# Kernel tuning notes

Hardware: AMD Instinct MI355X
Metric: run time of the kernel (lower is better)

## Reference

```python
import jax, jax.numpy as jnp
import numpy as np

B, S, D, H = 2, 2048, 768, 12
HD = D // H


def setup_inputs() -> dict:
    key = jax.random.key(0)
    ks = jax.random.split(key, 11)
    scale = 1.0 / np.sqrt(D)
    return {
        "query": jax.random.normal(ks[0], (B, S, D), jnp.float32),
        "key_": jax.random.normal(ks[1], (B, S, D), jnp.float32),
        "value": jax.random.normal(ks[2], (B, S, D), jnp.float32),
        "Wq": jax.random.normal(ks[3], (D, D), jnp.float32) * scale,
        "bq": jnp.zeros((D,), jnp.float32),
        "Wk": jax.random.normal(ks[4], (D, D), jnp.float32) * scale,
        "bk": jnp.zeros((D,), jnp.float32),
        "Wv": jax.random.normal(ks[5], (D, D), jnp.float32) * scale,
        "bv": jnp.zeros((D,), jnp.float32),
        "Wo": jax.random.normal(ks[6], (D, D), jnp.float32) * scale,
        "bo": jnp.zeros((D,), jnp.float32),
    }


def reference(query, key_, value, Wq, bq, Wk, bk, Wv, bv, Wo, bo):
    # Linear projections (W stored as [in, out]); dropout = identity (eval)
    def split_heads(x):
        # [B, S, D] -> [B, H, S, HD]
        return x.reshape(B, S, H, HD).transpose(0, 2, 1, 3)

    Q = split_heads(query @ Wq + bq)
    K = split_heads(key_ @ Wk + bk)
    V = split_heads(value @ Wv + bv)

    inv_sqrt_dk = 1.0 / jnp.sqrt(jnp.asarray(HD, Q.dtype))
    score = jnp.einsum("bhqd,bhkd->bhqk", Q, K) * inv_sqrt_dk  # [B,H,S,S]
    prob = jax.nn.softmax(score, axis=-1)  # source bug: mask is never applied
    out = jnp.einsum("bhqk,bhkd->bhqd", prob, V)  # [B,H,S,HD]
    out = out.transpose(0, 2, 1, 3).reshape(B, S, D)
    return out @ Wo + bo
```

## Files before the change

### kernel.cpp

```cpp
#include <hip/hip_runtime.h>
#include <hip/hip_bf16.h>

#define BB 2
#define SS 2048
#define DDIM 768
#define NH 12
#define HD 64
#define MTOT (BB*SS)

constexpr float QSCALE = 0.125f * 1.44269504088896340736f;

typedef __bf16 bf16_t;
typedef __bf16 bf16x8 __attribute__((ext_vector_type(8)));
typedef __bf16 bf16x4 __attribute__((ext_vector_type(4)));
typedef float  f32x4  __attribute__((ext_vector_type(4)));

static __device__ __forceinline__ f32x4 mfma16(bf16x8 a, bf16x8 b, f32x4 c) {
    return __builtin_amdgcn_mfma_f32_16x16x32_bf16(a, b, c, 0, 0, 0);
}

typedef __attribute__((address_space(3))) unsigned int lds_u32;
typedef __attribute__((address_space(1))) const unsigned int glob_u32;
static __device__ __forceinline__ void gload16(const bf16_t* g, bf16_t* l) {
    __builtin_amdgcn_global_load_lds((glob_u32*)g, (lds_u32*)l, 16, 0, 0);
}

__global__ __launch_bounds__(256) void prep_w(
    const float* __restrict__ Wq, const float* __restrict__ Wk,
    const float* __restrict__ Wv, const float* __restrict__ Wo,
    bf16_t* __restrict__ Wt)
{
    const int z = blockIdx.z, tid = threadIdx.x;
    __shared__ float tile[32][33];
    const float* W = (z == 0) ? Wq : (z == 1) ? Wk : (z == 2) ? Wv : Wo;
    int n0 = blockIdx.x * 32, k0 = blockIdx.y * 32;
    int tx = tid & 31, ty = tid >> 5;
#pragma unroll
    for (int i = 0; i < 4; i++) {
        int k = ty + i * 8;
        tile[k][tx] = W[(size_t)(k0 + k) * DDIM + n0 + tx];
    }
    __syncthreads();
    bf16_t* out = Wt + (size_t)z * DDIM * DDIM;
#pragma unroll
    for (int i = 0; i < 4; i++) {
        int n = ty + i * 8;
        out[(size_t)(n0 + n) * DDIM + k0 + tx] = (bf16_t)tile[tx][n];
    }
}

__global__ __launch_bounds__(256) void gemm_qkv(
    const float* __restrict__ qf32, const float* __restrict__ kf32,
    const float* __restrict__ vf,
    const float* __restrict__ bq, const float* __restrict__ bk, const float* __restrict__ bv,
    const bf16_t* __restrict__ Wt,
    bf16_t* __restrict__ Q, bf16_t* __restrict__ K, bf16_t* __restrict__ Vtg)
{
    __shared__ alignas(16) bf16_t As[128 * 64];
    __shared__ alignas(16) bf16_t Bs[128 * 64];
    const int z = blockIdx.z;
    const int m0 = blockIdx.y * 128, n0 = blockIdx.x * 128;
    const int tid = threadIdx.x, lane = tid & 63, w = tid >> 6;
    const int wm = (w >> 1) * 64, wn = (w & 1) * 64;
    const int quad = lane >> 4, l15 = lane & 15;

    const float* Af = (z == 0) ? qf32 : (z == 1) ? kf32 : vf;
    const bf16_t* Bt = Wt + (size_t)z * (DDIM * DDIM);
    const int arow = lane >> 3;
    const int asl  = ((lane & 7) ^ arow) * 8;
    bf16_t* BsW = &Bs[w * 2048];
    const int frow = tid >> 1, fhalf = tid & 1;

    f32x4 acc[4][4];
#pragma unroll
    for (int mt = 0; mt < 4; mt++)
#pragma unroll
        for (int nt = 0; nt < 4; nt++) { f32x4 zz = {0.f,0.f,0.f,0.f}; acc[mt][nt] = zz; }

    for (int k0 = 0; k0 < DDIM; k0 += 64) {
        __syncthreads();
        {
            const float* src = Af + (size_t)(m0 + frow) * DDIM + k0 + fhalf * 32;
            f32x4 v[8];
#pragma unroll
            for (int i = 0; i < 8; i++) v[i] = *(const f32x4*)(src + 4 * i);
            int rsw = frow & 7;
#pragma unroll
            for (int j = 0; j < 4; j++) {
                bf16x8 oj;
#pragma unroll
                for (int e = 0; e < 4; e++) {
                    oj[e]     = (bf16_t)v[2 * j][e];
                    oj[e + 4] = (bf16_t)v[2 * j + 1][e];
                }
                int phys = (fhalf * 4 + j) ^ rsw;
                *(bf16x8*)&As[frow * 64 + phys * 8] = oj;
            }
        }
        {
            const bf16_t* Bg = Bt + (size_t)(n0 + w * 32 + arow) * DDIM + k0 + asl;
#pragma unroll
            for (int i = 0; i < 4; i++)
                gload16(Bg + (size_t)(8 * i) * DDIM, BsW + 512 * i);
        }
        __syncthreads();

#pragma unroll
        for (int h = 0; h < 2; h++) {
            bf16x8 a[4], b[4];
#pragma unroll
            for (int mt = 0; mt < 4; mt++) {
                int r = wm + mt * 16 + l15;
                a[mt] = *(const bf16x8*)&As[r * 64 + (((h * 4 + quad) ^ (r & 7)) * 8)];
            }
#pragma unroll
            for (int nt = 0; nt < 4; nt++) {
                int r = wn + nt * 16 + l15;
                b[nt] = *(const bf16x8*)&Bs[r * 64 + (((h * 4 + quad) ^ (r & 7)) * 8)];
            }
#pragma unroll
            for (int mt = 0; mt < 4; mt++)
#pragma unroll
                for (int nt = 0; nt < 4; nt++)
                    acc[mt][nt] = mfma16(a[mt], b[nt], acc[mt][nt]);
        }
    }

    const float* bias = (z == 0) ? bq : (z == 1) ? bk : bv;
    float bvals[4];
#pragma unroll
    for (int nt = 0; nt < 4; nt++)
        bvals[nt] = bias[n0 + wn + nt * 16 + l15];

    if (z == 2) {
#pragma unroll
        for (int mt = 0; mt < 4; mt++) {
            int row0 = m0 + wm + mt * 16 + quad * 4;
#pragma unroll
            for (int nt = 0; nt < 4; nt++) {
                int col = n0 + wn + nt * 16 + l15;
                bf16x4 pk;
#pragma unroll
                for (int r = 0; r < 4; r++) pk[r] = (bf16_t)(acc[mt][nt][r] + bvals[nt]);
                *(bf16x4*)&Vtg[(size_t)col * MTOT + row0] = pk;
            }
        }
    } else {
        bf16_t* C = (z == 0) ? Q : K;
        float scale = (z == 0) ? QSCALE : 1.0f;
#pragma unroll
        for (int mt = 0; mt < 4; mt++) {
            int row0 = m0 + wm + mt * 16 + quad * 4;
#pragma unroll
            for (int nt = 0; nt < 4; nt++) {
                int col = n0 + wn + nt * 16 + l15;
#pragma unroll
                for (int r = 0; r < 4; r++)
                    C[(size_t)(row0 + r) * DDIM + col] = (bf16_t)((acc[mt][nt][r] + bvals[nt]) * scale);
            }
        }
    }
}

__global__ __launch_bounds__(256) void gemm_out(
    const bf16_t* __restrict__ Ab, const bf16_t* __restrict__ Bt,
    const float* __restrict__ bo, float* __restrict__ out)
{
    __shared__ alignas(16) bf16_t As[128 * 64];
    __shared__ alignas(16) bf16_t Bs[128 * 64];
    const int m0 = blockIdx.y * 128, n0 = blockIdx.x * 128;
    const int tid = threadIdx.x, lane = tid & 63, w = tid >> 6;
    const int wm = (w >> 1) * 64, wn = (w & 1) * 64;
    const int quad = lane >> 4, l15 = lane & 15;
    const int arow = lane >> 3;
    const int asl  = ((lane & 7) ^ arow) * 8;
    bf16_t* AsW = &As[w * 2048];
    bf16_t* BsW = &Bs[w * 2048];

    f32x4 acc[4][4];
#pragma unroll
    for (int mt = 0; mt < 4; mt++)
#pragma unroll
        for (int nt = 0; nt < 4; nt++) { f32x4 zz = {0.f,0.f,0.f,0.f}; acc[mt][nt] = zz; }

    for (int k0 = 0; k0 < DDIM; k0 += 64) {
        __syncthreads();
        {
            const bf16_t* Ag = Ab + (size_t)(m0 + w * 32 + arow) * DDIM + k0 + asl;
#pragma unroll
            for (int i = 0; i < 4; i++)
                gload16(Ag + (size_t)(8 * i) * DDIM, AsW + 512 * i);
            const bf16_t* Bg = Bt + (size_t)(n0 + w * 32 + arow) * DDIM + k0 + asl;
#pragma unroll
            for (int i = 0; i < 4; i++)
                gload16(Bg + (size_t)(8 * i) * DDIM, BsW + 512 * i);
        }
        __syncthreads();

#pragma unroll
        for (int h = 0; h < 2; h++) {
            bf16x8 a[4], b[4];
#pragma unroll
            for (int mt = 0; mt < 4; mt++) {
                int r = wm + mt * 16 + l15;
                a[mt] = *(const bf16x8*)&As[r * 64 + (((h * 4 + quad) ^ (r & 7)) * 8)];
            }
#pragma unroll
            for (int nt = 0; nt < 4; nt++) {
                int r = wn + nt * 16 + l15;
                b[nt] = *(const bf16x8*)&Bs[r * 64 + (((h * 4 + quad) ^ (r & 7)) * 8)];
            }
#pragma unroll
            for (int mt = 0; mt < 4; mt++)
#pragma unroll
                for (int nt = 0; nt < 4; nt++)
                    acc[mt][nt] = mfma16(a[mt], b[nt], acc[mt][nt]);
        }
    }

    float bvals[4];
#pragma unroll
    for (int nt = 0; nt < 4; nt++)
        bvals[nt] = bo[n0 + wn + nt * 16 + l15];
#pragma unroll
    for (int mt = 0; mt < 4; mt++) {
        int row0 = m0 + wm + mt * 16 + quad * 4;
#pragma unroll
        for (int nt = 0; nt < 4; nt++) {
            int col = n0 + wn + nt * 16 + l15;
#pragma unroll
            for (int r = 0; r < 4; r++)
                out[(size_t)(row0 + r) * DDIM + col] = acc[mt][nt][r] + bvals[nt];
        }
    }
}

__global__ __launch_bounds__(256) void attn_kernel(
    const bf16_t* __restrict__ Qb, const bf16_t* __restrict__ Kb,
    const bf16_t* __restrict__ Vtg, bf16_t* __restrict__ Ab)
{
    const int id = blockIdx.x;
    const int hb = id % 24, qi = id / 24;
    const int h = hb % NH, b = hb / NH;
    const int q0 = qi * 64;
    const int tid = threadIdx.x, lane = tid & 63, w = tid >> 6;
    const int quad = lane >> 4, l15 = lane & 15;

    __shared__ union {
        struct {
            alignas(16) bf16_t Ps[64][144];
        } a;
        struct {
            alignas(16) float Obuf[2][64][68];
            float Lb[4][64];
        } m;
    } u;

    bf16x8 qf[4][2];
#pragma unroll
    for (int qt = 0; qt < 4; qt++) {
        const bf16_t* src = Qb + (size_t)(b * SS + q0 + qt * 16 + l15) * DDIM + h * HD;
#pragma unroll
        for (int kh = 0; kh < 2; kh++)
            qf[qt][kh] = *(const bf16x8*)(src + kh * 32 + quad * 8);
    }

    f32x4 o[4][4];
#pragma unroll
    for (int dt = 0; dt < 4; dt++)
#pragma unroll
        for (int qt = 0; qt < 4; qt++) { f32x4 z = {0.f,0.f,0.f,0.f}; o[dt][qt] = z; }
    float l_s[4];
#pragma unroll
    for (int qt = 0; qt < 4; qt++) l_s[qt] = 0.f;

    const bf16_t* kfrag = Kb + (size_t)(b * SS + w * 32 + l15) * DDIM + h * HD + quad * 8;
    const bf16_t* vfrag = Vtg + (size_t)(h * HD + l15) * MTOT + b * SS + w * 32 + quad * 8;

    for (int kt0 = 0; kt0 < SS; kt0 += 128) {
        f32x4 s_[2][4];
#pragma unroll
        for (int kt = 0; kt < 2; kt++) {
            const bf16_t* kr = kfrag + (size_t)(kt0 + kt * 16) * DDIM;
            bf16x8 ak0 = *(const bf16x8*)(kr);
            bf16x8 ak1 = *(const bf16x8*)(kr + 32);
#pragma unroll
            for (int qt = 0; qt < 4; qt++) {
                f32x4 z = {0.f,0.f,0.f,0.f};
                z = mfma16(ak0, qf[qt][0], z);
                z = mfma16(ak1, qf[qt][1], z);
                s_[kt][qt] = z;
            }
        }

#pragma unroll
        for (int qt = 0; qt < 4; qt++) {
            float rs = l_s[qt];
#pragma unroll
            for (int kt = 0; kt < 2; kt++) {
                bf16x4 pk;
#pragma unroll
                for (int r = 0; r < 4; r++) {
                    float p = __builtin_amdgcn_exp2f(s_[kt][qt][r]);
                    rs += p;
                    pk[r] = (bf16_t)p;
                }
                *(bf16x4*)&u.a.Ps[qt * 16 + l15][w * 32 + kt * 16 + quad * 4] = pk;
            }
            l_s[qt] = rs;
        }

        bf16x8 av8[4], bp[4];
#pragma unroll
        for (int dt = 0; dt < 4; dt++)
            av8[dt] = *(const bf16x8*)(vfrag + (size_t)(dt * 16) * MTOT + kt0);
#pragma unroll
        for (int qt = 0; qt < 4; qt++)
            bp[qt] = *(const bf16x8*)&u.a.Ps[qt * 16 + l15][w * 32 + quad * 8];
#pragma unroll
        for (int dt = 0; dt < 4; dt++)
#pragma unroll
            for (int qt = 0; qt < 4; qt++)
                o[dt][qt] = mfma16(av8[dt], bp[qt], o[dt][qt]);
    }

#pragma unroll
    for (int qt = 0; qt < 4; qt++) {
        float rs = l_s[qt];
        rs += __shfl_xor(rs, 16, 64);
        rs += __shfl_xor(rs, 32, 64);
        l_s[qt] = rs;
    }
    __syncthreads();
    if (quad == 0) {
#pragma unroll
        for (int qt = 0; qt < 4; qt++)
            u.m.Lb[w][qt * 16 + l15] = l_s[qt];
    }
    __syncthreads();
    float lstar[4];
#pragma unroll
    for (int qt = 0; qt < 4; qt++) {
        int q = qt * 16 + l15;
        lstar[qt] = u.m.Lb[0][q] + u.m.Lb[1][q] + u.m.Lb[2][q] + u.m.Lb[3][q];
    }
    if (w >= 2) {
        float* dst = &u.m.Obuf[w - 2][lane][0];
#pragma unroll
        for (int dt = 0; dt < 4; dt++)
#pragma unroll
            for (int qt = 0; qt < 4; qt++)
                *(f32x4*)(dst + (dt * 4 + qt) * 4) = o[dt][qt];
    }
    __syncthreads();
    if (w < 2) {
        const float* src = &u.m.Obuf[w][lane][0];
#pragma unroll
        for (int dt = 0; dt < 4; dt++)
#pragma unroll
            for (int qt = 0; qt < 4; qt++)
                o[dt][qt] += *(const f32x4*)(src + (dt * 4 + qt) * 4);
    }
    __syncthreads();
    if (w == 1) {
        float* dst = &u.m.Obuf[0][lane][0];
#pragma unroll
        for (int dt = 0; dt < 4; dt++)
#pragma unroll
            for (int qt = 0; qt < 4; qt++)
                *(f32x4*)(dst + (dt * 4 + qt) * 4) = o[dt][qt];
    }
    __syncthreads();
    if (w == 0) {
        const float* src = &u.m.Obuf[0][lane][0];
#pragma unroll
        for (int dt = 0; dt < 4; dt++)
#pragma unroll
            for (int qt = 0; qt < 4; qt++)
                o[dt][qt] += *(const f32x4*)(src + (dt * 4 + qt) * 4);
#pragma unroll
        for (int qt = 0; qt < 4; qt++) {
            float inv = 1.f / lstar[qt];
            size_t rbase = (size_t)(b * SS + q0 + qt * 16 + l15) * DDIM + h * HD;
#pragma unroll
            for (int dt = 0; dt < 4; dt++) {
                bf16x4 pk;
#pragma unroll
                for (int r = 0; r < 4; r++) pk[r] = (bf16_t)(o[dt][qt][r] * inv);
                *(bf16x4*)&Ab[rbase + dt * 16 + quad * 4] = pk;
            }
        }
    }
}

extern "C" void kernel_launch(void* const* d_in, const int* in_sizes, int n_in,
                              void* d_out, int out_size, void* d_ws, size_t ws_size,
                              hipStream_t stream)
{
    const float* q  = (const float*)d_in[0];
    const float* k  = (const float*)d_in[1];
    const float* v  = (const float*)d_in[2];
    const float* Wq = (const float*)d_in[3];
    const float* bq = (const float*)d_in[4];
    const float* Wk = (const float*)d_in[5];
    const float* bk = (const float*)d_in[6];
    const float* Wv = (const float*)d_in[7];
    const float* bv = (const float*)d_in[8];
    const float* Wo = (const float*)d_in[9];
    const float* bo = (const float*)d_in[10];
    float* out = (float*)d_out;

    bf16_t* Wt  = (bf16_t*)d_ws;
    bf16_t* Ab  = Wt + (size_t)4 * DDIM * DDIM;
    bf16_t* Qs  = Ab + (size_t)MTOT * DDIM;
    bf16_t* Ks  = Qs + (size_t)MTOT * DDIM;
    bf16_t* Vtg = Ks + (size_t)MTOT * DDIM;

    prep_w<<<dim3(24, 24, 4), 256, 0, stream>>>(Wq, Wk, Wv, Wo, Wt);
    gemm_qkv<<<dim3(6, 32, 3), 256, 0, stream>>>(q, k, v, bq, bk, bv, Wt, Qs, Ks, Vtg);
    attn_kernel<<<dim3((SS / 64) * NH * BB), 256, 0, stream>>>(Qs, Ks, Vtg, Ab);
    gemm_out<<<dim3(6, 32), 256, 0, stream>>>(Ab, Wt + (size_t)3 * DDIM * DDIM, bo, out);
}
```

Baseline: 224.3 us.

## Shrink projection GEMM tiles, remap blocks across XCDs, prefetch fp32 A tiles

The QKV projection GEMM now uses 64x128 tiles, giving 1152 blocks instead of 576. The output GEMM uses 64x64 tiles, giving 768 blocks instead of 192. A block-index remap groups consecutive logical tiles onto the same XCD, which should improve L2 reuse. In the QKV kernel, the fp32 A loads for the next k-step are issued into registers before the MFMA loop so their latency overlaps compute. The aim is better CU occupancy and wave count on the MI355X, at the cost of less operand reuse per block and more redundant weight and activation loads.

Measured after the change: 197.9 us (median of 2 runs). -11.8%, faster.

```diff
diff --git a/kernel.cpp b/kernel.cpp
--- a/kernel.cpp
+++ b/kernel.cpp
@@ -56,12 +56,17 @@
     const bf16_t* __restrict__ Wt,
     bf16_t* __restrict__ Q, bf16_t* __restrict__ K, bf16_t* __restrict__ Vtg)
 {
-    __shared__ alignas(16) bf16_t As[128 * 64];
+    __shared__ alignas(16) bf16_t As[64 * 64];
     __shared__ alignas(16) bf16_t Bs[128 * 64];
-    const int z = blockIdx.z;
-    const int m0 = blockIdx.y * 128, n0 = blockIdx.x * 128;
+    const int gid = blockIdx.x;
+    const int lid = (gid & 7) * 144 + (gid >> 3);
+    const int z   = lid / 384;
+    const int rem = lid - z * 384;
+    const int mi  = rem / 6, ni = rem - mi * 6;
+    const int m0 = mi * 64, n0 = ni * 128;
+
     const int tid = threadIdx.x, lane = tid & 63, w = tid >> 6;
-    const int wm = (w >> 1) * 64, wn = (w & 1) * 64;
+    const int wm = (w >> 1) * 32, wn = (w & 1) * 64;
     const int quad = lane >> 4, l15 = lane & 15;
 
     const float* Af = (z == 0) ? qf32 : (z == 1) ? kf32 : vf;
@@ -69,33 +74,32 @@
     const int arow = lane >> 3;
     const int asl  = ((lane & 7) ^ arow) * 8;
     bf16_t* BsW = &Bs[w * 2048];
-    const int frow = tid >> 1, fhalf = tid & 1;
-
-    f32x4 acc[4][4];
-#pragma unroll
-    for (int mt = 0; mt < 4; mt++)
+    const int frow = tid >> 2, fq = tid & 3;
+    const int rsw = frow & 7;
+    const float* Abase = Af + (size_t)(m0 + frow) * DDIM + fq * 16;
+
+    f32x4 acc[2][4];
+#pragma unroll
+    for (int mt = 0; mt < 2; mt++)
 #pragma unroll
         for (int nt = 0; nt < 4; nt++) { f32x4 zz = {0.f,0.f,0.f,0.f}; acc[mt][nt] = zz; }
+
+    f32x4 vA[4];
+#pragma unroll
+    for (int i = 0; i < 4; i++) vA[i] = *(const f32x4*)(Abase + 4 * i);
 
     for (int k0 = 0; k0 < DDIM; k0 += 64) {
         __syncthreads();
-        {
-            const float* src = Af + (size_t)(m0 + frow) * DDIM + k0 + fhalf * 32;
-            f32x4 v[8];
-#pragma unroll
-            for (int i = 0; i < 8; i++) v[i] = *(const f32x4*)(src + 4 * i);
-            int rsw = frow & 7;
-#pragma unroll
-            for (int j = 0; j < 4; j++) {
-                bf16x8 oj;
-#pragma unroll
-                for (int e = 0; e < 4; e++) {
-                    oj[e]     = (bf16_t)v[2 * j][e];
-                    oj[e + 4] = (bf16_t)v[2 * j + 1][e];
-                }
-                int phys = (fhalf * 4 + j) ^ rsw;
-                *(bf16x8*)&As[frow * 64 + phys * 8] = oj;
-            }
+#pragma unroll
+        for (int j = 0; j < 2; j++) {
+            bf16x8 oj;
+#pragma unroll
+            for (int e = 0; e < 4; e++) {
+                oj[e]     = (bf16_t)vA[2 * j][e];
+                oj[e + 4] = (bf16_t)vA[2 * j + 1][e];
+            }
+            int phys = (fq * 2 + j) ^ rsw;
+            *(bf16x8*)&As[frow * 64 + phys * 8] = oj;
         }
         {
             const bf16_t* Bg = Bt + (size_t)(n0 + w * 32 + arow) * DDIM + k0 + asl;
@@ -104,12 +108,16 @@
                 gload16(Bg + (size_t)(8 * i) * DDIM, BsW + 512 * i);
         }
         __syncthreads();
-
+        if (k0 + 64 < DDIM) {
+            const float* nsrc = Abase + k0 + 64;
+#pragma unroll
+            for (int i = 0; i < 4; i++) vA[i] = *(const f32x4*)(nsrc + 4 * i);
+        }
 #pragma unroll
         for (int h = 0; h < 2; h++) {
-            bf16x8 a[4], b[4];
-#pragma unroll
-            for (int mt = 0; mt < 4; mt++) {
+            bf16x8 a[2], b[4];
+#pragma unroll
+            for (int mt = 0; mt < 2; mt++) {
                 int r = wm + mt * 16 + l15;
                 a[mt] = *(const bf16x8*)&As[r * 64 + (((h * 4 + quad) ^ (r & 7)) * 8)];
             }
@@ -119,7 +127,7 @@
                 b[nt] = *(const bf16x8*)&Bs[r * 64 + (((h * 4 + quad) ^ (r & 7)) * 8)];
             }
 #pragma unroll
-            for (int mt = 0; mt < 4; mt++)
+            for (int mt = 0; mt < 2; mt++)
 #pragma unroll
                 for (int nt = 0; nt < 4; nt++)
                     acc[mt][nt] = mfma16(a[mt], b[nt], acc[mt][nt]);
@@ -134,7 +142,7 @@
 
     if (z == 2) {
 #pragma unroll
-        for (int mt = 0; mt < 4; mt++) {
+        for (int mt = 0; mt < 2; mt++) {
             int row0 = m0 + wm + mt * 16 + quad * 4;
 #pragma unroll
             for (int nt = 0; nt < 4; nt++) {
@@ -149,7 +157,7 @@
         bf16_t* C = (z == 0) ? Q : K;
         float scale = (z == 0) ? QSCALE : 1.0f;
 #pragma unroll
-        for (int mt = 0; mt < 4; mt++) {
+        for (int mt = 0; mt < 2; mt++) {
             int row0 = m0 + wm + mt * 16 + quad * 4;
 #pragma unroll
             for (int nt = 0; nt < 4; nt++) {
@@ -166,67 +174,69 @@
     const bf16_t* __restrict__ Ab, const bf16_t* __restrict__ Bt,
     const float* __restrict__ bo, float* __restrict__ out)
 {
-    __shared__ alignas(16) bf16_t As[128 * 64];
-    __shared__ alignas(16) bf16_t Bs[128 * 64];
-    const int m0 = blockIdx.y * 128, n0 = blockIdx.x * 128;
+    __shared__ alignas(16) bf16_t As[64 * 64];
+    __shared__ alignas(16) bf16_t Bs[64 * 64];
+    const int gid = blockIdx.x;
+    const int lid = (gid & 7) * 96 + (gid >> 3);
+    const int mi  = lid / 12, ni = lid - mi * 12;
+    const int m0 = mi * 64, n0 = ni * 64;
+
     const int tid = threadIdx.x, lane = tid & 63, w = tid >> 6;
-    const int wm = (w >> 1) * 64, wn = (w & 1) * 64;
+    const int wm = (w >> 1) * 32, wn = (w & 1) * 32;
     const int quad = lane >> 4, l15 = lane & 15;
     const int arow = lane >> 3;
     const int asl  = ((lane & 7) ^ arow) * 8;
-    bf16_t* AsW = &As[w * 2048];
-    bf16_t* BsW = &Bs[w * 2048];
-
-    f32x4 acc[4][4];
-#pragma unroll
-    for (int mt = 0; mt < 4; mt++)
-#pragma unroll
-        for (int nt = 0; nt < 4; nt++) { f32x4 zz = {0.f,0.f,0.f,0.f}; acc[mt][nt] = zz; }
+    bf16_t* AsW = &As[w * 1024];
+    bf16_t* BsW = &Bs[w * 1024];
+
+    f32x4 acc[2][2];
+#pragma unroll
+    for (int mt = 0; mt < 2; mt++)
+#pragma unroll
+        for (int nt = 0; nt < 2; nt++) { f32x4 zz = {0.f,0.f,0.f,0.f}; acc[mt][nt] = zz; }
 
     for (int k0 = 0; k0 < DDIM; k0 += 64) {
         __syncthreads();
         {
-            const bf16_t* Ag = Ab + (size_t)(m0 + w * 32 + arow) * DDIM + k0 + asl;
-#pragma unroll
-            for (int i = 0; i < 4; i++)
-                gload16(Ag + (size_t)(8 * i) * DDIM, AsW + 512 * i);
-            const bf16_t* Bg = Bt + (size_t)(n0 + w * 32 + arow) * DDIM + k0 + asl;
-#pragma unroll
-            for (int i = 0; i < 4; i++)
-                gload16(Bg + (size_t)(8 * i) * DDIM, BsW + 512 * i);
+            const bf16_t* Ag = Ab + (size_t)(m0 + w * 16 + arow) * DDIM + k0 + asl;
+            gload16(Ag, AsW);
+            gload16(Ag + (size_t)8 * DDIM, AsW + 512);
+            const bf16_t* Bg = Bt + (size_t)(n0 + w * 16 + arow) * DDIM + k0 + asl;
+            gload16(Bg, BsW);
+            gload16(Bg + (size_t)8 * DDIM, BsW + 512);
         }
         __syncthreads();
 
 #pragma unroll
         for (int h = 0; h < 2; h++) {
-            bf16x8 a[4], b[4];
-#pragma unroll
-            for (int mt = 0; mt < 4; mt++) {
+            bf16x8 a[2], b[2];
+#pragma unroll
+            for (int mt = 0; mt < 2; mt++) {
                 int r = wm + mt * 16 + l15;
                 a[mt] = *(const bf16x8*)&As[r * 64 + (((h * 4 + quad) ^ (r & 7)) * 8)];
             }
 #pragma unroll
-            for (int nt = 0; nt < 4; nt++) {
+            for (int nt = 0; nt < 2; nt++) {
                 int r = wn + nt * 16 + l15;
                 b[nt] = *(const bf16x8*)&Bs[r * 64 + (((h * 4 + quad) ^ (r & 7)) * 8)];
             }
 #pragma unroll
-            for (int mt = 0; mt < 4; mt++)
-#pragma unroll
-                for (int nt = 0; nt < 4; nt++)
+            for (int mt = 0; mt < 2; mt++)
+#pragma unroll
+                for (int nt = 0; nt < 2; nt++)
                     acc[mt][nt] = mfma16(a[mt], b[nt], acc[mt][nt]);
         }
     }
 
-    float bvals[4];
-#pragma unroll
-    for (int nt = 0; nt < 4; nt++)
+    float bvals[2];
+#pragma unroll
+    for (int nt = 0; nt < 2; nt++)
         bvals[nt] = bo[n0 + wn + nt * 16 + l15];
 #pragma unroll
-    for (int mt = 0; mt < 4; mt++) {
+    for (int mt = 0; mt < 2; mt++) {
         int row0 = m0 + wm + mt * 16 + quad * 4;
 #pragma unroll
-        for (int nt = 0; nt < 4; nt++) {
+        for (int nt = 0; nt < 2; nt++) {
             int col = n0 + wn + nt * 16 + l15;
 #pragma unroll
             for (int r = 0; r < 4; r++)
@@ -417,7 +427,7 @@
     bf16_t* Vtg = Ks + (size_t)MTOT * DDIM;
 
     prep_w<<<dim3(24, 24, 4), 256, 0, stream>>>(Wq, Wk, Wv, Wo, Wt);
-    gemm_qkv<<<dim3(6, 32, 3), 256, 0, stream>>>(q, k, v, bq, bk, bv, Wt, Qs, Ks, Vtg);
+    gemm_qkv<<<dim3(1152), 256, 0, stream>>>(q, k, v, bq, bk, bv, Wt, Qs, Ks, Vtg);
     attn_kernel<<<dim3((SS / 64) * NH * BB), 256, 0, stream>>>(Qs, Ks, Vtg, Ab);
-    gemm_out<<<dim3(6, 32), 256, 0, stream>>>(Ab, Wt + (size_t)3 * DDIM * DDIM, bo, out);
-}
+    gemm_out<<<dim3(768), 256, 0, stream>>>(Ab, Wt + (size_t)3 * DDIM * DDIM, bo, out);
+}
```
